# Kernel optimization log

Hardware: AMD Instinct MI355X
Metric: run time of the kernel (lower is better)

## Reference

```python
import jax, jax.numpy as jnp
import numpy as np

N_NODES = 100000
N_EDGES = 1600000
D_IN = 128
D_OUT = 128


def setup_inputs() -> dict:
    key = jax.random.key(0)
    k1, k2, k3, k4, k5 = jax.random.split(key, 5)
    H = jax.random.normal(k1, (N_NODES, D_IN), dtype=jnp.float32)
    vals = jax.random.uniform(k2, (N_EDGES,), dtype=jnp.float32)
    W = jax.random.normal(k3, (D_OUT, D_IN), dtype=jnp.float32) * (1.0 / np.sqrt(D_IN))
    rows = jax.random.randint(k4, (N_EDGES,), 0, N_NODES, dtype=jnp.int32)
    cols = jax.random.randint(k5, (N_EDGES,), 0, N_NODES, dtype=jnp.int32)
    return {"H": H, "vals": vals, "W": W, "rows": rows, "cols": cols}


def reference(H, vals, W, rows, cols):
    # Single-rank: communicate_fgm is a no-op (X is zeros, no remote peers).
    # SpMM: out[i] = sum_e vals[e] * H[cols[e]] for edges with rows[e] == i
    msgs = vals[:, None] * H[cols]                      # [n_edges, d_in] irregular gather
    AH = jax.ops.segment_sum(msgs, rows, num_segments=N_NODES)  # [n_nodes, d_in]
    # Linear (no bias) + ReLU
    out = jax.nn.relu(AH @ W.T)                          # [n_nodes, d_out]
    return out
```

## Files before the change

### kernel.cpp

```cpp
#include <hip/hip_runtime.h>

#define N_NODES 100000
#define N_EDGES 1600000
#define D 128

#define NB 782
#define SLOT 2560
#define CHUNK 6400
#define NBLK_BUCKET 250

#define WB_OFF     0u
#define HWB_OFF    65536u
#define BCNT_OFF   25665536u
#define EPACK0_OFF 25669632u

typedef unsigned int uint;
typedef __attribute__((ext_vector_type(4))) float f32x4;
typedef __attribute__((ext_vector_type(8))) short bf16x8;

__device__ __forceinline__ unsigned short f2bf(float x) {
    uint u = __float_as_uint(x);
    uint r = u + 0x7fffu + ((u >> 16) & 1u);
    return (unsigned short)(r >> 16);
}

__device__ __forceinline__ void acc8(float acc[8], uint4 q, float v) {
    acc[0] = fmaf(v, __uint_as_float(q.x << 16),         acc[0]);
    acc[1] = fmaf(v, __uint_as_float(q.x & 0xffff0000u), acc[1]);
    acc[2] = fmaf(v, __uint_as_float(q.y << 16),         acc[2]);
    acc[3] = fmaf(v, __uint_as_float(q.y & 0xffff0000u), acc[3]);
    acc[4] = fmaf(v, __uint_as_float(q.z << 16),         acc[4]);
    acc[5] = fmaf(v, __uint_as_float(q.z & 0xffff0000u), acc[5]);
    acc[6] = fmaf(v, __uint_as_float(q.w << 16),         acc[6]);
    acc[7] = fmaf(v, __uint_as_float(q.w & 0xffff0000u), acc[7]);
}

__global__ void k_cast_w(const float* __restrict__ W, unsigned short* __restrict__ Wb) {
    int i = blockIdx.x * blockDim.x + threadIdx.x;
    Wb[i] = f2bf(W[i]);
}

__global__ __launch_bounds__(256) void k_gemm_mfma(const float* __restrict__ H,
                                                   const unsigned short* __restrict__ Wb,
                                                   unsigned short* __restrict__ HWb) {
    const int wave = threadIdx.x >> 6;
    const int lane = threadIdx.x & 63;
    const int rowtile = blockIdx.x * 4 + wave;
    if (rowtile >= N_NODES / 16) return;
    const int rowbase = rowtile * 16;
    const int m    = lane & 15;
    const int quad = lane >> 4;

    f32x4 acc[8];
    #pragma unroll
    for (int nt = 0; nt < 8; ++nt) acc[nt] = (f32x4){0.f, 0.f, 0.f, 0.f};

    const float* hrow = H + (size_t)(rowbase + m) * D;

    #pragma unroll
    for (int ks = 0; ks < 4; ++ks) {
        const int k0 = ks * 32 + quad * 8;
        float4 a0 = *(const float4*)(hrow + k0);
        float4 a1 = *(const float4*)(hrow + k0 + 4);
        bf16x8 afr;
        afr[0] = (short)f2bf(a0.x); afr[1] = (short)f2bf(a0.y);
        afr[2] = (short)f2bf(a0.z); afr[3] = (short)f2bf(a0.w);
        afr[4] = (short)f2bf(a1.x); afr[5] = (short)f2bf(a1.y);
        afr[6] = (short)f2bf(a1.z); afr[7] = (short)f2bf(a1.w);
        #pragma unroll
        for (int nt = 0; nt < 8; ++nt) {
            bf16x8 bfr = *(const bf16x8*)(Wb + (size_t)(nt * 16 + m) * D + k0);
            acc[nt] = __builtin_amdgcn_mfma_f32_16x16x32_bf16(afr, bfr, acc[nt], 0, 0, 0);
        }
    }

    #pragma unroll
    for (int nt = 0; nt < 8; ++nt) {
        #pragma unroll
        for (int r = 0; r < 4; ++r) {
            int orow = rowbase + quad * 4 + r;
            HWb[(size_t)orow * D + nt * 16 + m] = f2bf(acc[nt][r]);
        }
    }
}

__global__ __launch_bounds__(256) void k_bucket_coarse(const int* __restrict__ rows,
                                                       const int* __restrict__ cols,
                                                       const float* __restrict__ vals,
                                                       int* __restrict__ bcnt,
                                                       int2* __restrict__ epack0) {
    __shared__ int srows[CHUNK];
    __shared__ int hist[NB];
    __shared__ int cur[NB];
    const int tid = threadIdx.x;
    const int e0  = blockIdx.x * CHUNK;

    for (int b = tid; b < NB; b += 256) hist[b] = 0;
    __syncthreads();

    for (int i = tid; i < CHUNK; i += 256) {
        int r = rows[e0 + i];
        srows[i] = r;
        atomicAdd(&hist[r >> 7], 1);
    }
    __syncthreads();

    for (int b = tid; b < NB; b += 256) {
        int c = hist[b];
        int base = (c > 0) ? atomicAdd(&bcnt[b], c) : 0;
        cur[b] = b * SLOT + base;
    }
    __syncthreads();

    for (int i = tid; i < CHUNK; i += 256) {
        int r = srows[i];
        int b = r >> 7;
        int p = atomicAdd(&cur[b], 1);
        epack0[p] = make_int2(((r & 127) << 17) | cols[e0 + i],
                              __float_as_int(vals[e0 + i]));
    }
}

__global__ __launch_bounds__(256) void k_spmm_fused(const int* __restrict__ bcnt,
                                                    const int2* __restrict__ epack0,
                                                    const unsigned short* __restrict__ HWb,
                                                    float* __restrict__ out) {
    __shared__ int   scol[SLOT];
    __shared__ float sval[SLOT];
    __shared__ int hist[128];
    __shared__ int sc[128];
    __shared__ int cur[128];
    __shared__ int rstart[128];
    const int tid  = threadIdx.x;
    const int b    = blockIdx.x;
    const int base = b * SLOT;
    const int n_e  = bcnt[b];

    if (tid < 128) hist[tid] = 0;
    __syncthreads();

    for (int i = tid; i < n_e; i += 256)
        atomicAdd(&hist[epack0[base + i].x >> 17], 1);
    __syncthreads();

    if (tid < 128) sc[tid] = hist[tid];
    __syncthreads();
    #pragma unroll
    for (int off = 1; off < 128; off <<= 1) {
        int t = (tid < 128 && tid >= off) ? sc[tid - off] : 0;
        __syncthreads();
        if (tid < 128) sc[tid] += t;
        __syncthreads();
    }
    if (tid < 128) {
        int ex = sc[tid] - hist[tid];
        rstart[tid] = ex;
        cur[tid] = ex;
    }
    __syncthreads();

    for (int i = tid; i < n_e; i += 256) {
        int2 e  = epack0[base + i];
        int  lr = e.x >> 17;
        int  p  = atomicAdd(&cur[lr], 1);
        scol[p] = e.x & 0x1FFFF;
        sval[p] = __int_as_float(e.y);
    }
    __syncthreads();

    const int lane  = tid & 15;
    const int group = tid >> 4;

    #pragma unroll
    for (int rr = 0; rr < 8; ++rr) {
        const int lr  = group * 8 + rr;
        const int row = b * 128 + lr;
        if (row >= N_NODES) continue;
        const int s  = rstart[lr];
        const int e_ = cur[lr];

        float acc[8];
        #pragma unroll
        for (int c = 0; c < 8; ++c) acc[c] = 0.f;

        int j = s;
        for (; j + 3 < e_; j += 4) {
            int   c0 = scol[j],     c1 = scol[j + 1], c2 = scol[j + 2], c3 = scol[j + 3];
            float v0 = sval[j],     v1 = sval[j + 1], v2 = sval[j + 2], v3 = sval[j + 3];
            uint4 q0 = ((const uint4*)(HWb + (size_t)c0 * D))[lane];
            uint4 q1 = ((const uint4*)(HWb + (size_t)c1 * D))[lane];
            uint4 q2 = ((const uint4*)(HWb + (size_t)c2 * D))[lane];
            uint4 q3 = ((const uint4*)(HWb + (size_t)c3 * D))[lane];
            acc8(acc, q0, v0); acc8(acc, q1, v1);
            acc8(acc, q2, v2); acc8(acc, q3, v3);
        }
        for (; j < e_; ++j) {
            int   c = scol[j];
            float v = sval[j];
            uint4 q = ((const uint4*)(HWb + (size_t)c * D))[lane];
            acc8(acc, q, v);
        }

        float4 o0 = make_float4(fmaxf(acc[0], 0.f), fmaxf(acc[1], 0.f),
                                fmaxf(acc[2], 0.f), fmaxf(acc[3], 0.f));
        float4 o1 = make_float4(fmaxf(acc[4], 0.f), fmaxf(acc[5], 0.f),
                                fmaxf(acc[6], 0.f), fmaxf(acc[7], 0.f));
        ((float4*)out)[row * 32 + lane * 2]     = o0;
        ((float4*)out)[row * 32 + lane * 2 + 1] = o1;
    }
}

extern "C" void kernel_launch(void* const* d_in, const int* in_sizes, int n_in,
                              void* d_out, int out_size, void* d_ws, size_t ws_size,
                              hipStream_t stream) {
    const float* H    = (const float*)d_in[0];
    const float* vals = (const float*)d_in[1];
    const float* W    = (const float*)d_in[2];
    const int*   rows = (const int*)d_in[3];
    const int*   cols = (const int*)d_in[4];
    float* out = (float*)d_out;

    char* ws = (char*)d_ws;
    unsigned short* Wb     = (unsigned short*)(ws + WB_OFF);
    unsigned short* HWb    = (unsigned short*)(ws + HWB_OFF);
    int*            bcnt   = (int*)(ws + BCNT_OFF);
    int2*           epack0 = (int2*)(ws + EPACK0_OFF);

    k_cast_w<<<64, 256, 0, stream>>>(W, Wb);
    k_gemm_mfma<<<(N_NODES / 16 + 3) / 4, 256, 0, stream>>>(H, Wb, HWb);

    hipMemsetAsync(bcnt, 0, NB * sizeof(int), stream);
    k_bucket_coarse<<<NBLK_BUCKET, 256, 0, stream>>>(rows, cols, vals, bcnt, epack0);
    k_spmm_fused<<<NB, 256, 0, stream>>>(bcnt, epack0, HWb, out);
}
```

Baseline: 264.4 us.

## Phase SpMM gather by column range to improve L2 locality of HWb

Each bucket's edges are now sorted by (local row, column phase) instead of by row alone, with 8 column phases covering 12500 nodes each. All rows in a block walk phase by phase, so concurrent blocks tend to gather from the same slice of HWb at the same time, which should keep that slice resident in L2/MALL. In exchange each thread holds 64 float accumulators, which raises register pressure and may lower occupancy. The prefix scan also grows from 128 to 1024 entries, and the gather unroll drops from 4 to 2.

```diff
diff --git a/kernel.cpp b/kernel.cpp
--- a/kernel.cpp
+++ b/kernel.cpp
@@ -8,6 +8,9 @@
 #define SLOT 2560
 #define CHUNK 6400
 #define NBLK_BUCKET 250
+
+#define NPHASE 8
+#define COLS_PER_PHASE 12500
 
 #define WB_OFF     0u
 #define HWB_OFF    65536u
@@ -127,43 +130,55 @@
                                                     float* __restrict__ out) {
     __shared__ int   scol[SLOT];
     __shared__ float sval[SLOT];
-    __shared__ int hist[128];
-    __shared__ int sc[128];
-    __shared__ int cur[128];
-    __shared__ int rstart[128];
+    __shared__ int hist[1024];
+    __shared__ int cur[1024];
+    __shared__ int tsum[256];
     const int tid  = threadIdx.x;
     const int b    = blockIdx.x;
     const int base = b * SLOT;
     const int n_e  = bcnt[b];
 
-    if (tid < 128) hist[tid] = 0;
-    __syncthreads();
-
-    for (int i = tid; i < n_e; i += 256)
-        atomicAdd(&hist[epack0[base + i].x >> 17], 1);
-    __syncthreads();
-
-    if (tid < 128) sc[tid] = hist[tid];
-    __syncthreads();
-    #pragma unroll
-    for (int off = 1; off < 128; off <<= 1) {
-        int t = (tid < 128 && tid >= off) ? sc[tid - off] : 0;
-        __syncthreads();
-        if (tid < 128) sc[tid] += t;
-        __syncthreads();
-    }
-    if (tid < 128) {
-        int ex = sc[tid] - hist[tid];
-        rstart[tid] = ex;
-        cur[tid] = ex;
-    }
+    for (int i = tid; i < 1024; i += 256) hist[i] = 0;
     __syncthreads();
 
     for (int i = tid; i < n_e; i += 256) {
         int2 e  = epack0[base + i];
-        int  lr = e.x >> 17;
-        int  p  = atomicAdd(&cur[lr], 1);
-        scol[p] = e.x & 0x1FFFF;
+        int col = e.x & 0x1FFFF;
+        int key = ((e.x >> 17) << 3) | (col / COLS_PER_PHASE);
+        atomicAdd(&hist[key], 1);
+    }
+    __syncthreads();
+
+    int run = 0;
+    #pragma unroll
+    for (int k = 0; k < 4; ++k) {
+        int t2 = hist[tid * 4 + k];
+        hist[tid * 4 + k] = run;
+        run += t2;
+    }
+    tsum[tid] = run;
+    __syncthreads();
+    int myv = run;
+    #pragma unroll
+    for (int off = 1; off < 256; off <<= 1) {
+        int t2 = (tid >= off) ? tsum[tid - off] : 0;
+        __syncthreads();
+        tsum[tid] += t2;
+        __syncthreads();
+    }
+    int tbase = tsum[tid] - myv;
+    #pragma unroll
+    for (int k = 0; k < 4; ++k) hist[tid * 4 + k] += tbase;
+    __syncthreads();
+    for (int i = tid; i < 1024; i += 256) cur[i] = hist[i];
+    __syncthreads();
+
+    for (int i = tid; i < n_e; i += 256) {
+        int2 e  = epack0[base + i];
+        int col = e.x & 0x1FFFF;
+        int key = ((e.x >> 17) << 3) | (col / COLS_PER_PHASE);
+        int p   = atomicAdd(&cur[key], 1);
+        scol[p] = col;
         sval[p] = __int_as_float(e.y);
     }
     __syncthreads();
@@ -171,42 +186,46 @@
     const int lane  = tid & 15;
     const int group = tid >> 4;
 
+    float acc[8][8];
+    #pragma unroll
+    for (int rr = 0; rr < 8; ++rr)
+        #pragma unroll
+        for (int c = 0; c < 8; ++c) acc[rr][c] = 0.f;
+
+    for (int p = 0; p < NPHASE; ++p) {
+        #pragma unroll
+        for (int rr = 0; rr < 8; ++rr) {
+            const int key = ((group * 8 + rr) << 3) | p;
+            int j  = hist[key];
+            int e_ = cur[key];
+            for (; j + 1 < e_; j += 2) {
+                int   c0 = scol[j],     c1 = scol[j + 1];
+                float v0 = sval[j],     v1 = sval[j + 1];
+                uint4 q0 = ((const uint4*)(HWb + (size_t)c0 * D))[lane];
+                uint4 q1 = ((const uint4*)(HWb + (size_t)c1 * D))[lane];
+                acc8(acc[rr], q0, v0);
+                acc8(acc[rr], q1, v1);
+            }
+            if (j < e_) {
+                int   c = scol[j];
+                float v = sval[j];
+                uint4 q = ((const uint4*)(HWb + (size_t)c * D))[lane];
+                acc8(acc[rr], q, v);
+            }
+        }
+    }
+
     #pragma unroll
     for (int rr = 0; rr < 8; ++rr) {
-        const int lr  = group * 8 + rr;
-        const int row = b * 128 + lr;
-        if (row >= N_NODES) continue;
-        const int s  = rstart[lr];
-        const int e_ = cur[lr];
-
-        float acc[8];
-        #pragma unroll
-        for (int c = 0; c < 8; ++c) acc[c] = 0.f;
-
-        int j = s;
-        for (; j + 3 < e_; j += 4) {
-            int   c0 = scol[j],     c1 = scol[j + 1], c2 = scol[j + 2], c3 = scol[j + 3];
-            float v0 = sval[j],     v1 = sval[j + 1], v2 = sval[j + 2], v3 = sval[j + 3];
-            uint4 q0 = ((const uint4*)(HWb + (size_t)c0 * D))[lane];
-            uint4 q1 = ((const uint4*)(HWb + (size_t)c1 * D))[lane];
-            uint4 q2 = ((const uint4*)(HWb + (size_t)c2 * D))[lane];
-            uint4 q3 = ((const uint4*)(HWb + (size_t)c3 * D))[lane];
-            acc8(acc, q0, v0); acc8(acc, q1, v1);
-            acc8(acc, q2, v2); acc8(acc, q3, v3);
-        }
-        for (; j < e_; ++j) {
-            int   c = scol[j];
-            float v = sval[j];
-            uint4 q = ((const uint4*)(HWb + (size_t)c * D))[lane];
-            acc8(acc, q, v);
-        }
-
-        float4 o0 = make_float4(fmaxf(acc[0], 0.f), fmaxf(acc[1], 0.f),
-                                fmaxf(acc[2], 0.f), fmaxf(acc[3], 0.f));
-        float4 o1 = make_float4(fmaxf(acc[4], 0.f), fmaxf(acc[5], 0.f),
-                                fmaxf(acc[6], 0.f), fmaxf(acc[7], 0.f));
-        ((float4*)out)[row * 32 + lane * 2]     = o0;
-        ((float4*)out)[row * 32 + lane * 2 + 1] = o1;
+        const int row = b * 128 + group * 8 + rr;
+        if (row < N_NODES) {
+            float4 o0 = make_float4(fmaxf(acc[rr][0], 0.f), fmaxf(acc[rr][1], 0.f),
+                                    fmaxf(acc[rr][2], 0.f), fmaxf(acc[rr][3], 0.f));
+            float4 o1 = make_float4(fmaxf(acc[rr][4], 0.f), fmaxf(acc[rr][5], 0.f),
+                                    fmaxf(acc[rr][6], 0.f), fmaxf(acc[rr][7], 0.f));
+            ((float4*)out)[row * 32 + lane * 2]     = o0;
+            ((float4*)out)[row * 32 + lane * 2 + 1] = o1;
+        }
     }
 }
 
```

After: 276.3 us. +4.5%, slower.

## Fuse all stages into one persistent cooperative kernel with grid syncs

Applied to the files above, without the earlier changes.

Replaces the weight cast, memset, MFMA GEMM, bucketing and SpMM launches with a single cooperative kernel of 512 blocks that separates the phases with grid.sync. The GEMM output is now staged through LDS so HWb is written with coalesced 16-byte stores. The intent is to remove launch gaps and the memset, and to improve the GEMM store pattern. In exchange the grid is capped at 512 blocks, so each block loops over tiles and buckets, and grid-wide barriers plus 2-blocks-per-CU occupancy may limit latency hiding in the gather-heavy SpMM phase.

```diff
diff --git a/kernel.cpp b/kernel.cpp
--- a/kernel.cpp
+++ b/kernel.cpp
@@ -1,4 +1,5 @@
 #include <hip/hip_runtime.h>
+#include <hip/hip_cooperative_groups.h>
 
 #define N_NODES 100000
 #define N_EDGES 1600000
@@ -6,8 +7,9 @@
 
 #define NB 782
 #define SLOT 2560
-#define CHUNK 6400
-#define NBLK_BUCKET 250
+#define GRID 512
+#define CHUNK 3125
+#define NTILES 6250
 
 #define WB_OFF     0u
 #define HWB_OFF    65536u
@@ -17,6 +19,8 @@
 typedef unsigned int uint;
 typedef __attribute__((ext_vector_type(4))) float f32x4;
 typedef __attribute__((ext_vector_type(8))) short bf16x8;
+
+namespace cg = cooperative_groups;
 
 __device__ __forceinline__ unsigned short f2bf(float x) {
     uint u = __float_as_uint(x);
@@ -35,178 +39,197 @@
     acc[7] = fmaf(v, __uint_as_float(q.w & 0xffff0000u), acc[7]);
 }
 
-__global__ void k_cast_w(const float* __restrict__ W, unsigned short* __restrict__ Wb) {
-    int i = blockIdx.x * blockDim.x + threadIdx.x;
-    Wb[i] = f2bf(W[i]);
-}
-
-__global__ __launch_bounds__(256) void k_gemm_mfma(const float* __restrict__ H,
-                                                   const unsigned short* __restrict__ Wb,
-                                                   unsigned short* __restrict__ HWb) {
-    const int wave = threadIdx.x >> 6;
-    const int lane = threadIdx.x & 63;
-    const int rowtile = blockIdx.x * 4 + wave;
-    if (rowtile >= N_NODES / 16) return;
-    const int rowbase = rowtile * 16;
+union SMem {
+    unsigned short gtile[4][2048];
+    struct { int srows[CHUNK]; int hist[NB]; int cur[NB]; } bk;
+    struct { int scol[SLOT]; float sval[SLOT];
+             int hist[128], sc[128], cur[128], rstart[128]; } sp;
+};
+
+__global__ __launch_bounds__(256, 2) void k_fused(const float* __restrict__ H,
+                                                  const float* __restrict__ vals,
+                                                  const float* __restrict__ W,
+                                                  const int* __restrict__ rows,
+                                                  const int* __restrict__ cols,
+                                                  unsigned short* __restrict__ Wb,
+                                                  unsigned short* __restrict__ HWb,
+                                                  int* __restrict__ bcnt,
+                                                  int2* __restrict__ epack0,
+                                                  float* __restrict__ out) {
+    __shared__ SMem sm;
+    cg::grid_group grid = cg::this_grid();
+    const int tid = threadIdx.x;
+    const int b   = blockIdx.x;
+
+    {
+        int i = b * 256 + tid;
+        if (i < D * D) Wb[i] = f2bf(W[i]);
+        if (b == 64) {
+            for (int j = tid; j < NB; j += 256) bcnt[j] = 0;
+        }
+    }
+    __threadfence();
+    grid.sync();
+
+    const int wave = tid >> 6;
+    const int lane = tid & 63;
     const int m    = lane & 15;
     const int quad = lane >> 4;
 
-    f32x4 acc[8];
-    #pragma unroll
-    for (int nt = 0; nt < 8; ++nt) acc[nt] = (f32x4){0.f, 0.f, 0.f, 0.f};
-
-    const float* hrow = H + (size_t)(rowbase + m) * D;
-
-    #pragma unroll
-    for (int ks = 0; ks < 4; ++ks) {
-        const int k0 = ks * 32 + quad * 8;
-        float4 a0 = *(const float4*)(hrow + k0);
-        float4 a1 = *(const float4*)(hrow + k0 + 4);
-        bf16x8 afr;
-        afr[0] = (short)f2bf(a0.x); afr[1] = (short)f2bf(a0.y);
-        afr[2] = (short)f2bf(a0.z); afr[3] = (short)f2bf(a0.w);
-        afr[4] = (short)f2bf(a1.x); afr[5] = (short)f2bf(a1.y);
-        afr[6] = (short)f2bf(a1.z); afr[7] = (short)f2bf(a1.w);
+    for (int it = 0; it < 4; ++it) {
+        const int tile  = it * (GRID * 4) + b * 4 + wave;
+        const bool valid = (tile < NTILES);
+        if (valid) {
+            const int rowbase = tile * 16;
+            f32x4 acc[8];
+            #pragma unroll
+            for (int nt = 0; nt < 8; ++nt) acc[nt] = (f32x4){0.f, 0.f, 0.f, 0.f};
+
+            const float* hrow = H + (size_t)(rowbase + m) * D;
+            #pragma unroll
+            for (int ks = 0; ks < 4; ++ks) {
+                const int k0 = ks * 32 + quad * 8;
+                float4 a0 = *(const float4*)(hrow + k0);
+                float4 a1 = *(const float4*)(hrow + k0 + 4);
+                bf16x8 afr;
+                afr[0] = (short)f2bf(a0.x); afr[1] = (short)f2bf(a0.y);
+                afr[2] = (short)f2bf(a0.z); afr[3] = (short)f2bf(a0.w);
+                afr[4] = (short)f2bf(a1.x); afr[5] = (short)f2bf(a1.y);
+                afr[6] = (short)f2bf(a1.z); afr[7] = (short)f2bf(a1.w);
+                #pragma unroll
+                for (int nt = 0; nt < 8; ++nt) {
+                    bf16x8 bfr = *(const bf16x8*)(Wb + (size_t)(nt * 16 + m) * D + k0);
+                    acc[nt] = __builtin_amdgcn_mfma_f32_16x16x32_bf16(afr, bfr, acc[nt], 0, 0, 0);
+                }
+            }
+            unsigned short* lds = sm.gtile[wave];
+            #pragma unroll
+            for (int nt = 0; nt < 8; ++nt)
+                #pragma unroll
+                for (int r = 0; r < 4; ++r)
+                    lds[(quad * 4 + r) * 128 + nt * 16 + m] = f2bf(acc[nt][r]);
+        }
+        __syncthreads();
+        if (valid) {
+            const int rowbase = tile * 16;
+            const unsigned short* lds = sm.gtile[wave];
+            #pragma unroll
+            for (int c = 0; c < 4; ++c) {
+                int chunk = c * 64 + lane;
+                int row   = chunk >> 4;
+                int off   = chunk & 15;
+                uint4 q = *(const uint4*)(lds + row * 128 + off * 8);
+                *(uint4*)(HWb + (size_t)(rowbase + row) * D + off * 8) = q;
+            }
+        }
+        __syncthreads();
+    }
+
+    {
+        const int e0 = b * CHUNK;
+        for (int i = tid; i < NB; i += 256) sm.bk.hist[i] = 0;
+        __syncthreads();
+        for (int i = tid; i < CHUNK; i += 256) {
+            int r = rows[e0 + i];
+            sm.bk.srows[i] = r;
+            atomicAdd(&sm.bk.hist[r >> 7], 1);
+        }
+        __syncthreads();
+        for (int bb = tid; bb < NB; bb += 256) {
+            int c = sm.bk.hist[bb];
+            int base = (c > 0) ? atomicAdd(&bcnt[bb], c) : 0;
+            sm.bk.cur[bb] = bb * SLOT + base;
+        }
+        __syncthreads();
+        for (int i = tid; i < CHUNK; i += 256) {
+            int r = sm.bk.srows[i];
+            int p = atomicAdd(&sm.bk.cur[r >> 7], 1);
+            epack0[p] = make_int2(((r & 127) << 17) | cols[e0 + i],
+                                  __float_as_int(vals[e0 + i]));
+        }
+    }
+    __threadfence();
+    grid.sync();
+
+    const int lane16 = tid & 15;
+    const int group  = tid >> 4;
+
+    for (int bb = b; bb < NB; bb += GRID) {
+        const int base = bb * SLOT;
+        const int n_e  = bcnt[bb];
+
+        if (tid < 128) sm.sp.hist[tid] = 0;
+        __syncthreads();
+
+        for (int i = tid; i < n_e; i += 256)
+            atomicAdd(&sm.sp.hist[epack0[base + i].x >> 17], 1);
+        __syncthreads();
+
+        if (tid < 128) sm.sp.sc[tid] = sm.sp.hist[tid];
+        __syncthreads();
         #pragma unroll
-        for (int nt = 0; nt < 8; ++nt) {
-            bf16x8 bfr = *(const bf16x8*)(Wb + (size_t)(nt * 16 + m) * D + k0);
-            acc[nt] = __builtin_amdgcn_mfma_f32_16x16x32_bf16(afr, bfr, acc[nt], 0, 0, 0);
-        }
-    }
-
-    #pragma unroll
-    for (int nt = 0; nt < 8; ++nt) {
+        for (int off = 1; off < 128; off <<= 1) {
+            int t = (tid < 128 && tid >= off) ? sm.sp.sc[tid - off] : 0;
+            __syncthreads();
+            if (tid < 128) sm.sp.sc[tid] += t;
+            __syncthreads();
+        }
+        if (tid < 128) {
+            int ex = sm.sp.sc[tid] - sm.sp.hist[tid];
+            sm.sp.rstart[tid] = ex;
+            sm.sp.cur[tid]    = ex;
+        }
+        __syncthreads();
+
+        for (int i = tid; i < n_e; i += 256) {
+            int2 e  = epack0[base + i];
+            int  lr = e.x >> 17;
+            int  p  = atomicAdd(&sm.sp.cur[lr], 1);
+            sm.sp.scol[p] = e.x & 0x1FFFF;
+            sm.sp.sval[p] = __int_as_float(e.y);
+        }
+        __syncthreads();
+
         #pragma unroll
-        for (int r = 0; r < 4; ++r) {
-            int orow = rowbase + quad * 4 + r;
-            HWb[(size_t)orow * D + nt * 16 + m] = f2bf(acc[nt][r]);
-        }
-    }
-}
-
-__global__ __launch_bounds__(256) void k_bucket_coarse(const int* __restrict__ rows,
-                                                       const int* __restrict__ cols,
-                                                       const float* __restrict__ vals,
-                                                       int* __restrict__ bcnt,
-                                                       int2* __restrict__ epack0) {
-    __shared__ int srows[CHUNK];
-    __shared__ int hist[NB];
-    __shared__ int cur[NB];
-    const int tid = threadIdx.x;
-    const int e0  = blockIdx.x * CHUNK;
-
-    for (int b = tid; b < NB; b += 256) hist[b] = 0;
-    __syncthreads();
-
-    for (int i = tid; i < CHUNK; i += 256) {
-        int r = rows[e0 + i];
-        srows[i] = r;
-        atomicAdd(&hist[r >> 7], 1);
-    }
-    __syncthreads();
-
-    for (int b = tid; b < NB; b += 256) {
-        int c = hist[b];
-        int base = (c > 0) ? atomicAdd(&bcnt[b], c) : 0;
-        cur[b] = b * SLOT + base;
-    }
-    __syncthreads();
-
-    for (int i = tid; i < CHUNK; i += 256) {
-        int r = srows[i];
-        int b = r >> 7;
-        int p = atomicAdd(&cur[b], 1);
-        epack0[p] = make_int2(((r & 127) << 17) | cols[e0 + i],
-                              __float_as_int(vals[e0 + i]));
-    }
-}
-
-__global__ __launch_bounds__(256) void k_spmm_fused(const int* __restrict__ bcnt,
-                                                    const int2* __restrict__ epack0,
-                                                    const unsigned short* __restrict__ HWb,
-                                                    float* __restrict__ out) {
-    __shared__ int   scol[SLOT];
-    __shared__ float sval[SLOT];
-    __shared__ int hist[128];
-    __shared__ int sc[128];
-    __shared__ int cur[128];
-    __shared__ int rstart[128];
-    const int tid  = threadIdx.x;
-    const int b    = blockIdx.x;
-    const int base = b * SLOT;
-    const int n_e  = bcnt[b];
-
-    if (tid < 128) hist[tid] = 0;
-    __syncthreads();
-
-    for (int i = tid; i < n_e; i += 256)
-        atomicAdd(&hist[epack0[base + i].x >> 17], 1);
-    __syncthreads();
-
-    if (tid < 128) sc[tid] = hist[tid];
-    __syncthreads();
-    #pragma unroll
-    for (int off = 1; off < 128; off <<= 1) {
-        int t = (tid < 128 && tid >= off) ? sc[tid - off] : 0;
-        __syncthreads();
-        if (tid < 128) sc[tid] += t;
-        __syncthreads();
-    }
-    if (tid < 128) {
-        int ex = sc[tid] - hist[tid];
-        rstart[tid] = ex;
-        cur[tid] = ex;
-    }
-    __syncthreads();
-
-    for (int i = tid; i < n_e; i += 256) {
-        int2 e  = epack0[base + i];
-        int  lr = e.x >> 17;
-        int  p  = atomicAdd(&cur[lr], 1);
-        scol[p] = e.x & 0x1FFFF;
-        sval[p] = __int_as_float(e.y);
-    }
-    __syncthreads();
-
-    const int lane  = tid & 15;
-    const int group = tid >> 4;
-
-    #pragma unroll
-    for (int rr = 0; rr < 8; ++rr) {
-        const int lr  = group * 8 + rr;
-        const int row = b * 128 + lr;
-        if (row >= N_NODES) continue;
-        const int s  = rstart[lr];
-        const int e_ = cur[lr];
-
-        float acc[8];
-        #pragma unroll
-        for (int c = 0; c < 8; ++c) acc[c] = 0.f;
-
-        int j = s;
-        for (; j + 3 < e_; j += 4) {
-            int   c0 = scol[j],     c1 = scol[j + 1], c2 = scol[j + 2], c3 = scol[j + 3];
-            float v0 = sval[j],     v1 = sval[j + 1], v2 = sval[j + 2], v3 = sval[j + 3];
-            uint4 q0 = ((const uint4*)(HWb + (size_t)c0 * D))[lane];
-            uint4 q1 = ((const uint4*)(HWb + (size_t)c1 * D))[lane];
-            uint4 q2 = ((const uint4*)(HWb + (size_t)c2 * D))[lane];
-            uint4 q3 = ((const uint4*)(HWb + (size_t)c3 * D))[lane];
-            acc8(acc, q0, v0); acc8(acc, q1, v1);
-            acc8(acc, q2, v2); acc8(acc, q3, v3);
-        }
-        for (; j < e_; ++j) {
-            int   c = scol[j];
-            float v = sval[j];
-            uint4 q = ((const uint4*)(HWb + (size_t)c * D))[lane];
-            acc8(acc, q, v);
-        }
-
-        float4 o0 = make_float4(fmaxf(acc[0], 0.f), fmaxf(acc[1], 0.f),
-                                fmaxf(acc[2], 0.f), fmaxf(acc[3], 0.f));
-        float4 o1 = make_float4(fmaxf(acc[4], 0.f), fmaxf(acc[5], 0.f),
-                                fmaxf(acc[6], 0.f), fmaxf(acc[7], 0.f));
-        ((float4*)out)[row * 32 + lane * 2]     = o0;
-        ((float4*)out)[row * 32 + lane * 2 + 1] = o1;
+        for (int rr = 0; rr < 8; ++rr) {
+            const int lr  = group * 8 + rr;
+            const int row = bb * 128 + lr;
+            if (row >= N_NODES) continue;
+            const int s  = sm.sp.rstart[lr];
+            const int e_ = sm.sp.cur[lr];
+
+            float acc[8];
+            #pragma unroll
+            for (int c = 0; c < 8; ++c) acc[c] = 0.f;
+
+            int j = s;
+            for (; j + 3 < e_; j += 4) {
+                int   c0 = sm.sp.scol[j],     c1 = sm.sp.scol[j + 1];
+                int   c2 = sm.sp.scol[j + 2], c3 = sm.sp.scol[j + 3];
+                float v0 = sm.sp.sval[j],     v1 = sm.sp.sval[j + 1];
+                float v2 = sm.sp.sval[j + 2], v3 = sm.sp.sval[j + 3];
+                uint4 q0 = ((const uint4*)(HWb + (size_t)c0 * D))[lane16];
+                uint4 q1 = ((const uint4*)(HWb + (size_t)c1 * D))[lane16];
+                uint4 q2 = ((const uint4*)(HWb + (size_t)c2 * D))[lane16];
+                uint4 q3 = ((const uint4*)(HWb + (size_t)c3 * D))[lane16];
+                acc8(acc, q0, v0); acc8(acc, q1, v1);
+                acc8(acc, q2, v2); acc8(acc, q3, v3);
+            }
+            for (; j < e_; ++j) {
+                int   c = sm.sp.scol[j];
+                float v = sm.sp.sval[j];
+                uint4 q = ((const uint4*)(HWb + (size_t)c * D))[lane16];
+                acc8(acc, q, v);
+            }
+
+            float4 o0 = make_float4(fmaxf(acc[0], 0.f), fmaxf(acc[1], 0.f),
+                                    fmaxf(acc[2], 0.f), fmaxf(acc[3], 0.f));
+            float4 o1 = make_float4(fmaxf(acc[4], 0.f), fmaxf(acc[5], 0.f),
+                                    fmaxf(acc[6], 0.f), fmaxf(acc[7], 0.f));
+            ((float4*)out)[row * 32 + lane16 * 2]     = o0;
+            ((float4*)out)[row * 32 + lane16 * 2 + 1] = o1;
+        }
+        __syncthreads();
     }
 }
 
@@ -218,7 +241,7 @@
     const float* W    = (const float*)d_in[2];
     const int*   rows = (const int*)d_in[3];
     const int*   cols = (const int*)d_in[4];
-    float* out = (float*)d_out;
+    float* outp = (float*)d_out;
 
     char* ws = (char*)d_ws;
     unsigned short* Wb     = (unsigned short*)(ws + WB_OFF);
@@ -226,10 +249,7 @@
     int*            bcnt   = (int*)(ws + BCNT_OFF);
     int2*           epack0 = (int2*)(ws + EPACK0_OFF);
 
-    k_cast_w<<<64, 256, 0, stream>>>(W, Wb);
-    k_gemm_mfma<<<(N_NODES / 16 + 3) / 4, 256, 0, stream>>>(H, Wb, HWb);
-
-    hipMemsetAsync(bcnt, 0, NB * sizeof(int), stream);
-    k_bucket_coarse<<<NBLK_BUCKET, 256, 0, stream>>>(rows, cols, vals, bcnt, epack0);
-    k_spmm_fused<<<NB, 256, 0, stream>>>(bcnt, epack0, HWb, out);
-}
+    void* kargs[] = {(void*)&H, (void*)&vals, (void*)&W, (void*)&rows, (void*)&cols,
+                     (void*)&Wb, (void*)&HWb, (void*)&bcnt, (void*)&epack0, (void*)&outp};
+    hipLaunchCooperativeKernel((void*)k_fused, dim3(GRID), dim3(256), kargs, 0, stream);
+}
```

New measurement: 459.3 us. 1.74x slower.
